# Performance work log

Hardware: AMD Instinct MI355X
Metric: run time of the kernel (lower is better)

The kernel has to match this reference:

```python
import jax, jax.numpy as jnp
import numpy as np

HEAD_DIM = 64
N_HEADS = 16


def _rope_tables(seq_len, head_dim):
    pos = np.arange(seq_len, dtype=np.float32)
    freq = np.arange(0, head_dim, 2, dtype=np.float32) / head_dim
    inv_freq = 1.0 / (10000.0 ** freq)
    angles = np.outer(pos, inv_freq)                     # [S, D/2]
    angles = np.repeat(angles, 2, axis=-1)               # [S, D] interleaved
    return jnp.asarray(np.cos(angles)), jnp.asarray(np.sin(angles))


def _rotate_half(x):
    x1 = x[..., ::2]
    x2 = x[..., 1::2]
    return jnp.stack((-x2, x1), axis=-1).reshape(x.shape)


def _apply_rope(x, cos, sin):
    # x: [B, H, S, D]; cos/sin: [S, D]
    return x * cos + _rotate_half(x) * sin


def setup_inputs() -> dict:
    key = jax.random.key(0)
    ks = jax.random.split(key, 5)
    d = N_HEADS * HEAD_DIM
    B, S = 4, 2048
    s = 1.0 / np.sqrt(d)
    return {
        "x": jax.random.normal(ks[0], (B, S, d), dtype=jnp.float32),
        "Wq": jax.random.normal(ks[1], (d, d), dtype=jnp.float32) * s,
        "bq": jnp.zeros((d,), jnp.float32),
        "Wk": jax.random.normal(ks[2], (d, d), dtype=jnp.float32) * s,
        "bk": jnp.zeros((d,), jnp.float32),
        "Wv": jax.random.normal(ks[3], (d, d), dtype=jnp.float32) * s,
        "bv": jnp.zeros((d,), jnp.float32),
        "Wo": jax.random.normal(ks[4], (d, d), dtype=jnp.float32) * s,
        "bo": jnp.zeros((d,), jnp.float32),
    }


def reference(x, Wq, bq, Wk, bk, Wv, bv, Wo, bo):
    B, S, d = x.shape
    H, D = N_HEADS, HEAD_DIM
    scale = D ** -0.5

    q = (x @ Wq + bq).reshape(B, S, H, D).transpose(0, 2, 1, 3)  # [B,H,S,D]
    k = (x @ Wk + bk).reshape(B, S, H, D).transpose(0, 2, 1, 3)
    v = (x @ Wv + bv).reshape(B, S, H, D).transpose(0, 2, 1, 3)

    cos, sin = _rope_tables(S, D)
    q = _apply_rope(q, cos, sin)
    k = _apply_rope(k, cos, sin)

    att = jnp.einsum("bhqd,bhkd->bhqk", q, k) * scale            # [B,H,S,S]
    causal = jnp.tril(jnp.ones((S, S), dtype=bool))
    att = jnp.where(causal, att, -jnp.inf)
    att = jax.nn.softmax(att, axis=-1)

    y = jnp.einsum("bhqk,bhkd->bhqd", att, v)                    # [B,H,S,D]
    y = y.transpose(0, 2, 1, 3).reshape(B, S, d)
    return y @ Wo + bo
```

## Files before the change

kernel.cpp:

```cpp
#include <hip/hip_runtime.h>

typedef __bf16 bf16;
typedef __bf16 bf16x2 __attribute__((ext_vector_type(2)));
typedef __bf16 bf16x8 __attribute__((ext_vector_type(8)));
typedef float  f32x4  __attribute__((ext_vector_type(4)));

#define MFMA16(a,b,c) __builtin_amdgcn_mfma_f32_16x16x32_bf16(a,b,c,0,0,0)
#define GLL16(g, l) __builtin_amdgcn_global_load_lds( \
    (const __attribute__((address_space(1))) unsigned char*)(g), \
    (__attribute__((address_space(3))) unsigned char*)(l), 16, 0, 0)

constexpr int SEQ   = 2048;
constexpr int NH    = 16;
constexpr int HD    = 64;
constexpr int BATCH = 4;
constexpr int DM    = 1024;
constexpr int ROWS  = BATCH * SEQ;
constexpr size_t TEN = (size_t)BATCH * NH * SEQ * HD;

__global__ __launch_bounds__(256) void k_convert_x(const float* __restrict__ x,
                                                   bf16* __restrict__ xb) {
    size_t idx = ((size_t)blockIdx.x * 256 + threadIdx.x) * 8;
    float4 f0 = *(const float4*)(x + idx);
    float4 f1 = *(const float4*)(x + idx + 4);
    bf16x8 o;
    o[0] = (bf16)f0.x; o[1] = (bf16)f0.y; o[2] = (bf16)f0.z; o[3] = (bf16)f0.w;
    o[4] = (bf16)f1.x; o[5] = (bf16)f1.y; o[6] = (bf16)f1.z; o[7] = (bf16)f1.w;
    *(bf16x8*)(xb + idx) = o;
}

__global__ __launch_bounds__(256) void k_wtrans(const float* __restrict__ W0,
                                                const float* __restrict__ W1,
                                                const float* __restrict__ W2,
                                                const float* __restrict__ W3,
                                                bf16* __restrict__ Wt_all) {
    __shared__ float T[64][65];
    const int z = blockIdx.z;
    const float* W = (z == 0) ? W0 : (z == 1) ? W1 : (z == 2) ? W2 : W3;
    bf16* Wt = Wt_all + (size_t)z * DM * DM;
    const int t = threadIdx.x;
    const int kb = blockIdx.x, nb = blockIdx.y;
    const int rl = t >> 2, seg = t & 3;
    const float* src = W + (size_t)(kb * 64 + rl) * DM + nb * 64 + seg * 16;
#pragma unroll
    for (int j4 = 0; j4 < 4; j4++) {
        float4 f = *(const float4*)(src + j4 * 4);
        T[rl][seg * 16 + j4 * 4 + 0] = f.x;
        T[rl][seg * 16 + j4 * 4 + 1] = f.y;
        T[rl][seg * 16 + j4 * 4 + 2] = f.z;
        T[rl][seg * 16 + j4 * 4 + 3] = f.w;
    }
    __syncthreads();
    bf16* dst = Wt + (size_t)(nb * 64 + rl) * DM + kb * 64 + seg * 16;
    bf16x8 o0, o1;
#pragma unroll
    for (int j = 0; j < 8; j++) {
        o0[j] = (bf16)T[seg * 16 + j][rl];
        o1[j] = (bf16)T[seg * 16 + 8 + j][rl];
    }
    *(bf16x8*)dst = o0;
    *(bf16x8*)(dst + 8) = o1;
}

template <int MODE>
__global__ __launch_bounds__(256) void k_gemm(const bf16* __restrict__ A,
                                              const bf16* __restrict__ Wt0,
                                              const float* __restrict__ b0,
                                              const float* __restrict__ b1,
                                              const float* __restrict__ b2,
                                              void* __restrict__ out) {
    __shared__ __align__(1024) bf16 AsF[128 * 32];
    __shared__ __align__(1024) bf16 BsF[128 * 32];
    const int z = blockIdx.z;
    const bf16* Wt = Wt0 + (size_t)z * DM * DM;
    const float* bias = (z == 0) ? b0 : (z == 1) ? b1 : b2;

    const int t = threadIdx.x;
    const int w = t >> 6, lane = t & 63, quad = lane >> 4, l16 = lane & 15;
    const int bm = blockIdx.x * 128, bn = blockIdx.y * 128;
    const int wm = (w >> 1) * 64, wn = (w & 1) * 64;

    const int c0 = w * 2, c1 = w * 2 + 1;
    const int sg0 = c0 * 64 + lane, sg1 = c1 * 64 + lane;
    const int r0 = sg0 >> 2, r1 = sg1 >> 2;
    const int csg0 = (sg0 & 3) ^ ((r0 >> 1) & 3);
    const int csg1 = (sg1 & 3) ^ ((r1 >> 1) & 3);
    const bf16* gA0 = A  + (size_t)(bm + r0) * DM + csg0 * 8;
    const bf16* gA1 = A  + (size_t)(bm + r1) * DM + csg1 * 8;
    const bf16* gB0 = Wt + (size_t)(bn + r0) * DM + csg0 * 8;
    const bf16* gB1 = Wt + (size_t)(bn + r1) * DM + csg1 * 8;
    bf16* lA0 = AsF + c0 * 512;
    bf16* lA1 = AsF + c1 * 512;
    bf16* lB0 = BsF + c0 * 512;
    bf16* lB1 = BsF + c1 * 512;

    const bf16* pA[4]; const bf16* pB[4];
#pragma unroll
    for (int mt = 0; mt < 4; mt++) {
        const int r = wm + mt * 16 + l16;
        pA[mt] = AsF + r * 32 + ((quad ^ ((r >> 1) & 3)) << 3);
    }
#pragma unroll
    for (int nt = 0; nt < 4; nt++) {
        const int r = wn + nt * 16 + l16;
        pB[nt] = BsF + r * 32 + ((quad ^ ((r >> 1) & 3)) << 3);
    }

    f32x4 zero = {0.f, 0.f, 0.f, 0.f};
    f32x4 acc[4][4];
#pragma unroll
    for (int mt = 0; mt < 4; mt++)
#pragma unroll
        for (int nt = 0; nt < 4; nt++) acc[mt][nt] = zero;

    for (int k0 = 0; k0 < DM; k0 += 32) {
        __syncthreads();
        GLL16(gA0, lA0);
        GLL16(gA1, lA1);
        GLL16(gB0, lB0);
        GLL16(gB1, lB1);
        gA0 += 32; gA1 += 32; gB0 += 32; gB1 += 32;
        __syncthreads();

        bf16x8 af[4], bfr[4];
#pragma unroll
        for (int mt = 0; mt < 4; mt++) af[mt]  = *(const bf16x8*)pA[mt];
#pragma unroll
        for (int nt = 0; nt < 4; nt++) bfr[nt] = *(const bf16x8*)pB[nt];
#pragma unroll
        for (int mt = 0; mt < 4; mt++)
#pragma unroll
            for (int nt = 0; nt < 4; nt++)
                acc[mt][nt] = MFMA16(af[mt], bfr[nt], acc[mt][nt]);
    }

    float bv[4];
#pragma unroll
    for (int nt = 0; nt < 4; nt++) bv[nt] = bias[bn + wn + nt * 16 + l16];

#pragma unroll
    for (int mt = 0; mt < 4; mt++) {
#pragma unroll
        for (int nt = 0; nt < 4; nt++) {
            const int col = bn + wn + nt * 16 + l16;
#pragma unroll
            for (int rg = 0; rg < 4; rg++) {
                const int row = bm + wm + mt * 16 + quad * 4 + rg;
                const float val = acc[mt][nt][rg] + bv[nt];
                if (MODE == 0) {
                    const int b = row >> 11, s = row & (SEQ - 1);
                    const int h = col >> 6, dd = col & 63;
                    ((bf16*)out)[(size_t)z * TEN +
                                 (((size_t)(b * NH + h)) * SEQ + s) * HD + dd] = (bf16)val;
                } else {
                    ((float*)out)[(size_t)row * DM + col] = val;
                }
            }
        }
    }
}

__global__ __launch_bounds__(256) void k_rope(bf16* __restrict__ q, bf16* __restrict__ k) {
    const int tid = blockIdx.x * 256 + threadIdx.x;
    const int i  = tid & 31;
    const int s  = (tid >> 5) & (SEQ - 1);
    const int bh = tid >> 16;
    const size_t base = ((size_t)bh * SEQ + s) * HD + 2 * i;
    const float inv_freq = expf(-(float)i * 0.28782313662425574f);
    const float ang = (float)s * inv_freq;
    float sn, cs;
    sincosf(ang, &sn, &cs);
    bf16x2 qv = *(bf16x2*)(q + base);
    bf16x2 kv = *(bf16x2*)(k + base);
    const float q0 = (float)qv[0], q1 = (float)qv[1];
    const float k0 = (float)kv[0], k1 = (float)kv[1];
    bf16x2 qo, ko;
    qo[0] = (bf16)((q0 * cs - q1 * sn) * 0.125f);
    qo[1] = (bf16)((q1 * cs + q0 * sn) * 0.125f);
    ko[0] = (bf16)(k0 * cs - k1 * sn);
    ko[1] = (bf16)(k1 * cs + k0 * sn);
    *(bf16x2*)(q + base) = qo;
    *(bf16x2*)(k + base) = ko;
}

__global__ __launch_bounds__(256) void k_vtrans(const bf16* __restrict__ v, bf16* __restrict__ vt) {
    __shared__ float T[64][65];
    const int t = threadIdx.x;
    const int sb = blockIdx.x, bh = blockIdx.y;
    const int rl = t >> 2, seg = t & 3;
    const bf16* src = v + ((size_t)bh * SEQ + sb * 64 + rl) * HD + seg * 16;
    bf16x8 i0 = *(const bf16x8*)src;
    bf16x8 i1 = *(const bf16x8*)(src + 8);
#pragma unroll
    for (int j = 0; j < 8; j++) {
        T[rl][seg * 16 + j]     = (float)i0[j];
        T[rl][seg * 16 + 8 + j] = (float)i1[j];
    }
    __syncthreads();
    bf16* dst = vt + ((size_t)bh * HD + rl) * SEQ + sb * 64 + seg * 16;
    bf16x8 o0, o1;
#pragma unroll
    for (int j = 0; j < 8; j++) {
        o0[j] = (bf16)T[seg * 16 + j][rl];
        o1[j] = (bf16)T[seg * 16 + 8 + j][rl];
    }
    *(bf16x8*)dst = o0;
    *(bf16x8*)(dst + 8) = o1;
}

__global__ __launch_bounds__(256, 4) void k_attn(const bf16* __restrict__ q,
                                                 const bf16* __restrict__ k,
                                                 const bf16* __restrict__ vt,
                                                 bf16* __restrict__ y) {
    __shared__ __align__(16) bf16 Ks[64][72];
    __shared__ __align__(16) bf16 Vs[64][72];
    __shared__ __align__(16) bf16 Ps[4][16][72];
    const int t = threadIdx.x;
    const int w = t >> 6, lane = t & 63, quad = lane >> 4, l16 = lane & 15;
    const int bh = blockIdx.x;
    const int x  = blockIdx.y;
    const int b = bh >> 4, h = bh & 15;
    const int srow = t >> 3, sseg = t & 7;

    const bf16* kbase = k  + (size_t)bh * SEQ * HD;
    const bf16* vbase = vt + (size_t)bh * HD * SEQ;
    const float NEG_INF = -__builtin_inff();

#pragma unroll 1
    for (int pass = 0; pass < 2; pass++) {
        const int qt = pass ? x : 31 - x;

        const bf16* qrow = q + ((size_t)bh * SEQ + qt * 64 + w * 16 + l16) * HD;
        const bf16x8 qf0 = *(const bf16x8*)(qrow + quad * 8);
        const bf16x8 qf1 = *(const bf16x8*)(qrow + 32 + quad * 8);

        f32x4 zero = {0.f, 0.f, 0.f, 0.f};
        f32x4 minus10 = {-10.f, -10.f, -10.f, -10.f};
        f32x4 acc_o[4];
        float l_acc[4];
#pragma unroll
        for (int nt = 0; nt < 4; nt++) acc_o[nt] = zero;
#pragma unroll
        for (int rg = 0; rg < 4; rg++) l_acc[rg] = 0.f;

        for (int kt = 0; kt <= qt; kt++) {
            const bf16* kg = kbase + ((size_t)(kt * 64) + srow) * HD + sseg * 8;
            const bf16x8 kst0 = *(const bf16x8*)kg;
            const bf16x8 kst1 = *(const bf16x8*)(kg + 32 * HD);
            const bf16* vg = vbase + (size_t)srow * SEQ + kt * 64 + sseg * 8;
            const bf16x8 vst0 = *(const bf16x8*)vg;
            const bf16x8 vst1 = *(const bf16x8*)(vg + 32 * SEQ);
            __syncthreads();
            *(bf16x8*)&Ks[srow][sseg * 8]      = kst0;
            *(bf16x8*)&Ks[srow + 32][sseg * 8] = kst1;
            *(bf16x8*)&Vs[srow][sseg * 8]      = vst0;
            *(bf16x8*)&Vs[srow + 32][sseg * 8] = vst1;
            __syncthreads();

            f32x4 accs[4];
#pragma unroll
            for (int nt = 0; nt < 4; nt++) {
                const bf16x8 kf0 = *(const bf16x8*)&Ks[nt * 16 + l16][quad * 8];
                const bf16x8 kf1 = *(const bf16x8*)&Ks[nt * 16 + l16][32 + quad * 8];
                f32x4 a = minus10;
                a = MFMA16(qf0, kf0, a);
                a = MFMA16(qf1, kf1, a);
                accs[nt] = a;
            }
            if (kt == qt) {
#pragma unroll
                for (int nt = 0; nt < 4; nt++) {
                    const int kv = nt * 16 + l16;
#pragma unroll
                    for (int rg = 0; rg < 4; rg++) {
                        const int qr = w * 16 + quad * 4 + rg;
                        if (kv > qr) accs[nt][rg] = NEG_INF;
                    }
                }
            }
#pragma unroll
            for (int nt = 0; nt < 4; nt++) {
#pragma unroll
                for (int rg = 0; rg < 4; rg++) {
                    const float p = __expf(accs[nt][rg]);
                    accs[nt][rg] = p;
                    l_acc[rg] += p;
                }
            }
#pragma unroll
            for (int nt = 0; nt < 4; nt++) {
#pragma unroll
                for (int rg = 0; rg < 4; rg++)
                    Ps[w][quad * 4 + rg][nt * 16 + l16] = (bf16)accs[nt][rg];
            }
            const bf16x8 pf0 = *(const bf16x8*)&Ps[w][l16][quad * 8];
            const bf16x8 pf1 = *(const bf16x8*)&Ps[w][l16][32 + quad * 8];
#pragma unroll
            for (int nt = 0; nt < 4; nt++) {
                const bf16x8 vf0 = *(const bf16x8*)&Vs[nt * 16 + l16][quad * 8];
                const bf16x8 vf1 = *(const bf16x8*)&Vs[nt * 16 + l16][32 + quad * 8];
                acc_o[nt] = MFMA16(pf0, vf0, acc_o[nt]);
                acc_o[nt] = MFMA16(pf1, vf1, acc_o[nt]);
            }
        }

#pragma unroll
        for (int rg = 0; rg < 4; rg++) {
            float rs = l_acc[rg];
            rs += __shfl_xor(rs, 1);
            rs += __shfl_xor(rs, 2);
            rs += __shfl_xor(rs, 4);
            rs += __shfl_xor(rs, 8);
            const float inv = 1.0f / rs;
            const int s = qt * 64 + w * 16 + quad * 4 + rg;
#pragma unroll
            for (int nt = 0; nt < 4; nt++) {
                const float val = acc_o[nt][rg] * inv;
                y[((size_t)(b * SEQ + s)) * DM + h * HD + nt * 16 + l16] = (bf16)val;
            }
        }
    }
}

extern "C" void kernel_launch(void* const* d_in, const int* in_sizes, int n_in,
                              void* d_out, int out_size, void* d_ws, size_t ws_size,
                              hipStream_t stream) {
    const float* x  = (const float*)d_in[0];
    const float* Wq = (const float*)d_in[1];
    const float* bq = (const float*)d_in[2];
    const float* Wk = (const float*)d_in[3];
    const float* bk = (const float*)d_in[4];
    const float* Wv = (const float*)d_in[5];
    const float* bv = (const float*)d_in[6];
    const float* Wo = (const float*)d_in[7];
    const float* bo = (const float*)d_in[8];

    char* ws = (char*)d_ws;
    bf16* xb   = (bf16*)(ws);
    bf16* wall = (bf16*)(ws + (16ull << 20));
    bf16* qb   = (bf16*)(ws + (24ull << 20));
    bf16* kb   = (bf16*)(ws + (40ull << 20));
    bf16* vb   = (bf16*)(ws + (56ull << 20));
    bf16* vtb  = (bf16*)(ws + (72ull << 20));
    bf16* wot  = wall + 3ull * DM * DM;

    k_convert_x<<<4096, 256, 0, stream>>>(x, xb);
    k_wtrans<<<dim3(16, 16, 4), 256, 0, stream>>>(Wq, Wk, Wv, Wo, wall);
    k_gemm<0><<<dim3(64, 8, 3), 256, 0, stream>>>(xb, wall, bq, bk, bv, qb);
    k_rope<<<16384, 256, 0, stream>>>(qb, kb);
    k_vtrans<<<dim3(32, 64), 256, 0, stream>>>(vb, vtb);
    k_attn<<<dim3(64, 16), 256, 0, stream>>>(qb, kb, vtb, xb);
    k_gemm<1><<<dim3(64, 8, 1), 256, 0, stream>>>(xb, wot, bo, bo, bo, d_out);
}
```

Before: 278.7 us.

## Enlarge attention query tile to 128 rows with swizzled LDS and direct global-to-LDS loads

```diff
diff --git a/kernel.cpp b/kernel.cpp
--- a/kernel.cpp
+++ b/kernel.cpp
@@ -208,115 +208,165 @@
     *(bf16x8*)(dst + 8) = o1;
 }
 
-__global__ __launch_bounds__(256, 4) void k_attn(const bf16* __restrict__ q,
+__global__ __launch_bounds__(256, 2) void k_attn(const bf16* __restrict__ q,
                                                  const bf16* __restrict__ k,
                                                  const bf16* __restrict__ vt,
                                                  bf16* __restrict__ y) {
-    __shared__ __align__(16) bf16 Ks[64][72];
-    __shared__ __align__(16) bf16 Vs[64][72];
-    __shared__ __align__(16) bf16 Ps[4][16][72];
+    __shared__ __align__(1024) bf16 KsF[64 * 64];
+    __shared__ __align__(1024) bf16 VsF[64 * 64];
+    __shared__ __align__(1024) bf16 PsF[4 * 32 * 64];
     const int t = threadIdx.x;
     const int w = t >> 6, lane = t & 63, quad = lane >> 4, l16 = lane & 15;
     const int bh = blockIdx.x;
     const int x  = blockIdx.y;
     const int b = bh >> 4, h = bh & 15;
-    const int srow = t >> 3, sseg = t & 7;
+
+    const int srow = lane >> 3;
+    const int gseg = (lane & 7) ^ srow;
+    const int c0 = w, c1 = w + 4;
 
     const bf16* kbase = k  + (size_t)bh * SEQ * HD;
     const bf16* vbase = vt + (size_t)bh * HD * SEQ;
     const float NEG_INF = -__builtin_inff();
 
+    const bf16 *kf_p[4][2], *vf_p[4][2], *pf_p[2][2];
+#pragma unroll
+    for (int nt = 0; nt < 4; nt++) {
+        const int r = nt * 16 + l16;
+#pragma unroll
+        for (int hh = 0; hh < 2; hh++) {
+            const int sg = hh * 4 + quad;
+            kf_p[nt][hh] = KsF + r * 64 + (((sg ^ (r & 7))) << 3);
+            vf_p[nt][hh] = VsF + r * 64 + (((sg ^ (r & 7))) << 3);
+        }
+    }
+#pragma unroll
+    for (int mt = 0; mt < 2; mt++) {
+        const int r = mt * 16 + l16;
+#pragma unroll
+        for (int hh = 0; hh < 2; hh++) {
+            const int sg = hh * 4 + quad;
+            pf_p[mt][hh] = PsF + w * 2048 + r * 64 + (((sg ^ (r & 7))) << 3);
+        }
+    }
+
 #pragma unroll 1
     for (int pass = 0; pass < 2; pass++) {
-        const int qt = pass ? x : 31 - x;
-
-        const bf16* qrow = q + ((size_t)bh * SEQ + qt * 64 + w * 16 + l16) * HD;
-        const bf16x8 qf0 = *(const bf16x8*)(qrow + quad * 8);
-        const bf16x8 qf1 = *(const bf16x8*)(qrow + 32 + quad * 8);
+        const int qb = pass ? x : 15 - x;
+
+        bf16x8 qf[2][2];
+#pragma unroll
+        for (int mt = 0; mt < 2; mt++) {
+            const bf16* qrow = q + ((size_t)bh * SEQ + qb * 128 + w * 32 + mt * 16 + l16) * HD;
+            qf[mt][0] = *(const bf16x8*)(qrow + quad * 8);
+            qf[mt][1] = *(const bf16x8*)(qrow + 32 + quad * 8);
+        }
 
         f32x4 zero = {0.f, 0.f, 0.f, 0.f};
         f32x4 minus10 = {-10.f, -10.f, -10.f, -10.f};
-        f32x4 acc_o[4];
-        float l_acc[4];
-#pragma unroll
-        for (int nt = 0; nt < 4; nt++) acc_o[nt] = zero;
-#pragma unroll
-        for (int rg = 0; rg < 4; rg++) l_acc[rg] = 0.f;
-
-        for (int kt = 0; kt <= qt; kt++) {
-            const bf16* kg = kbase + ((size_t)(kt * 64) + srow) * HD + sseg * 8;
-            const bf16x8 kst0 = *(const bf16x8*)kg;
-            const bf16x8 kst1 = *(const bf16x8*)(kg + 32 * HD);
-            const bf16* vg = vbase + (size_t)srow * SEQ + kt * 64 + sseg * 8;
-            const bf16x8 vst0 = *(const bf16x8*)vg;
-            const bf16x8 vst1 = *(const bf16x8*)(vg + 32 * SEQ);
+        f32x4 acc_o[2][4];
+        float l_acc[2][4];
+#pragma unroll
+        for (int mt = 0; mt < 2; mt++)
+#pragma unroll
+            for (int nt = 0; nt < 4; nt++) acc_o[mt][nt] = zero;
+#pragma unroll
+        for (int mt = 0; mt < 2; mt++)
+#pragma unroll
+            for (int rg = 0; rg < 4; rg++) l_acc[mt][rg] = 0.f;
+
+        const bf16* kg0 = kbase + (size_t)(c0 * 8 + srow) * HD + gseg * 8;
+        const bf16* kg1 = kbase + (size_t)(c1 * 8 + srow) * HD + gseg * 8;
+        const bf16* vg0 = vbase + (size_t)(c0 * 8 + srow) * SEQ + gseg * 8;
+        const bf16* vg1 = vbase + (size_t)(c1 * 8 + srow) * SEQ + gseg * 8;
+        const int ktmax = 2 * qb + 1;
+
+        for (int kt = 0; kt <= ktmax; kt++) {
             __syncthreads();
-            *(bf16x8*)&Ks[srow][sseg * 8]      = kst0;
-            *(bf16x8*)&Ks[srow + 32][sseg * 8] = kst1;
-            *(bf16x8*)&Vs[srow][sseg * 8]      = vst0;
-            *(bf16x8*)&Vs[srow + 32][sseg * 8] = vst1;
+            GLL16(kg0, KsF + c0 * 512);
+            GLL16(kg1, KsF + c1 * 512);
+            GLL16(vg0, VsF + c0 * 512);
+            GLL16(vg1, VsF + c1 * 512);
+            kg0 += 64 * HD; kg1 += 64 * HD; vg0 += 64; vg1 += 64;
             __syncthreads();
 
-            f32x4 accs[4];
-#pragma unroll
-            for (int nt = 0; nt < 4; nt++) {
-                const bf16x8 kf0 = *(const bf16x8*)&Ks[nt * 16 + l16][quad * 8];
-                const bf16x8 kf1 = *(const bf16x8*)&Ks[nt * 16 + l16][32 + quad * 8];
-                f32x4 a = minus10;
-                a = MFMA16(qf0, kf0, a);
-                a = MFMA16(qf1, kf1, a);
-                accs[nt] = a;
+            const int d = qb * 128 + w * 32 - kt * 64;
+            if (d > -32) {
+                f32x4 accs[2][4];
+#pragma unroll
+                for (int nt = 0; nt < 4; nt++) {
+                    const bf16x8 kf0 = *(const bf16x8*)kf_p[nt][0];
+                    const bf16x8 kf1 = *(const bf16x8*)kf_p[nt][1];
+#pragma unroll
+                    for (int mt = 0; mt < 2; mt++) {
+                        f32x4 a = minus10;
+                        a = MFMA16(qf[mt][0], kf0, a);
+                        a = MFMA16(qf[mt][1], kf1, a);
+                        accs[mt][nt] = a;
+                    }
+                }
+                if (d < 64) {
+#pragma unroll
+                    for (int mt = 0; mt < 2; mt++) {
+                        const int qr = d + mt * 16 + quad * 4;
+#pragma unroll
+                        for (int nt = 0; nt < 4; nt++) {
+                            const int kv = nt * 16 + l16;
+#pragma unroll
+                            for (int rg = 0; rg < 4; rg++)
+                                if (kv > qr + rg) accs[mt][nt][rg] = NEG_INF;
+                        }
+                    }
+                }
+#pragma unroll
+                for (int mt = 0; mt < 2; mt++) {
+#pragma unroll
+                    for (int nt = 0; nt < 4; nt++) {
+#pragma unroll
+                        for (int rg = 0; rg < 4; rg++) {
+                            const float p = __expf(accs[mt][nt][rg]);
+                            l_acc[mt][rg] += p;
+                            const int prow = mt * 16 + quad * 4 + rg;
+                            const int psg  = (nt * 2 + (l16 >> 3)) ^ (prow & 7);
+                            PsF[w * 2048 + prow * 64 + psg * 8 + (l16 & 7)] = (bf16)p;
+                        }
+                    }
+                }
+                bf16x8 pf[2][2];
+#pragma unroll
+                for (int mt = 0; mt < 2; mt++) {
+                    pf[mt][0] = *(const bf16x8*)pf_p[mt][0];
+                    pf[mt][1] = *(const bf16x8*)pf_p[mt][1];
+                }
+#pragma unroll
+                for (int nt = 0; nt < 4; nt++) {
+                    const bf16x8 vf0 = *(const bf16x8*)vf_p[nt][0];
+                    const bf16x8 vf1 = *(const bf16x8*)vf_p[nt][1];
+#pragma unroll
+                    for (int mt = 0; mt < 2; mt++) {
+                        acc_o[mt][nt] = MFMA16(pf[mt][0], vf0, acc_o[mt][nt]);
+                        acc_o[mt][nt] = MFMA16(pf[mt][1], vf1, acc_o[mt][nt]);
+                    }
+                }
             }
-            if (kt == qt) {
+        }
+
+#pragma unroll
+        for (int mt = 0; mt < 2; mt++) {
+#pragma unroll
+            for (int rg = 0; rg < 4; rg++) {
+                float rs = l_acc[mt][rg];
+                rs += __shfl_xor(rs, 1);
+                rs += __shfl_xor(rs, 2);
+                rs += __shfl_xor(rs, 4);
+                rs += __shfl_xor(rs, 8);
+                const float inv = 1.0f / rs;
+                const int s = qb * 128 + w * 32 + mt * 16 + quad * 4 + rg;
 #pragma unroll
                 for (int nt = 0; nt < 4; nt++) {
-                    const int kv = nt * 16 + l16;
-#pragma unroll
-                    for (int rg = 0; rg < 4; rg++) {
-                        const int qr = w * 16 + quad * 4 + rg;
-                        if (kv > qr) accs[nt][rg] = NEG_INF;
-                    }
-                }
-            }
-#pragma unroll
-            for (int nt = 0; nt < 4; nt++) {
-#pragma unroll
-                for (int rg = 0; rg < 4; rg++) {
-                    const float p = __expf(accs[nt][rg]);
-                    accs[nt][rg] = p;
-                    l_acc[rg] += p;
-                }
-            }
-#pragma unroll
-            for (int nt = 0; nt < 4; nt++) {
-#pragma unroll
-                for (int rg = 0; rg < 4; rg++)
-                    Ps[w][quad * 4 + rg][nt * 16 + l16] = (bf16)accs[nt][rg];
-            }
-            const bf16x8 pf0 = *(const bf16x8*)&Ps[w][l16][quad * 8];
-            const bf16x8 pf1 = *(const bf16x8*)&Ps[w][l16][32 + quad * 8];
-#pragma unroll
-            for (int nt = 0; nt < 4; nt++) {
-                const bf16x8 vf0 = *(const bf16x8*)&Vs[nt * 16 + l16][quad * 8];
-                const bf16x8 vf1 = *(const bf16x8*)&Vs[nt * 16 + l16][32 + quad * 8];
-                acc_o[nt] = MFMA16(pf0, vf0, acc_o[nt]);
-                acc_o[nt] = MFMA16(pf1, vf1, acc_o[nt]);
-            }
-        }
-
-#pragma unroll
-        for (int rg = 0; rg < 4; rg++) {
-            float rs = l_acc[rg];
-            rs += __shfl_xor(rs, 1);
-            rs += __shfl_xor(rs, 2);
-            rs += __shfl_xor(rs, 4);
-            rs += __shfl_xor(rs, 8);
-            const float inv = 1.0f / rs;
-            const int s = qt * 64 + w * 16 + quad * 4 + rg;
-#pragma unroll
-            for (int nt = 0; nt < 4; nt++) {
-                const float val = acc_o[nt][rg] * inv;
-                y[((size_t)(b * SEQ + s)) * DM + h * HD + nt * 16 + l16] = (bf16)val;
+                    const float val = acc_o[mt][nt][rg] * inv;
+                    y[((size_t)(b * SEQ + s)) * DM + h * HD + nt * 16 + l16] = (bf16)val;
+                }
             }
         }
     }
@@ -349,6 +399,6 @@
     k_gemm<0><<<dim3(64, 8, 3), 256, 0, stream>>>(xb, wall, bq, bk, bv, qb);
     k_rope<<<16384, 256, 0, stream>>>(qb, kb);
     k_vtrans<<<dim3(32, 64), 256, 0, stream>>>(vb, vtb);
-    k_attn<<<dim3(64, 16), 256, 0, stream>>>(qb, kb, vtb, xb);
+    k_attn<<<dim3(64, 8), 256, 0, stream>>>(qb, kb, vtb, xb);
     k_gemm<1><<<dim3(64, 8, 1), 256, 0, stream>>>(xb, wot, bo, bo, bo, d_out);
 }
```

Result: faster. 266.7 us (-4.3%).
